# Kernel optimization log

Measured on AMD Instinct MI355X. Metric: run time of the kernel, lower is better.

Reference implementation:

```python
import jax, jax.numpy as jnp
import numpy as np

N_NODES = 100000
N_EDGES = 1600000
IN_FEAT = 64
HIDDEN = 128
N_CLASSES = 16
N_GRAPHS = 512


def _glorot(key, shape):
    fan_in, fan_out = shape
    lim = (6.0 / (fan_in + fan_out)) ** 0.5
    return jax.random.uniform(key, shape, jnp.float32, -lim, lim)


def setup_inputs() -> dict:
    key = jax.random.key(0)
    ks = jax.random.split(key, 12)
    x = jax.random.normal(ks[0], (N_NODES, IN_FEAT), jnp.float32)
    edge_index = jax.random.randint(ks[1], (2, N_EDGES), 0, N_NODES, jnp.int64)
    batch = jnp.sort(jax.random.randint(ks[2], (N_NODES,), 0, N_GRAPHS, jnp.int64))
    # SAGEConv params: lin_l (neighbor agg, with bias), lin_r (root, no bias)
    params = {}
    dims = [(IN_FEAT, HIDDEN), (HIDDEN, HIDDEN), (HIDDEN, HIDDEN)]
    for i, (din, dout) in enumerate(dims, start=1):
        params[f"Wl{i}"] = _glorot(ks[2 + 2 * i - 1], (din, dout))
        params[f"bl{i}"] = jnp.zeros((dout,), jnp.float32)
        params[f"Wr{i}"] = _glorot(ks[2 + 2 * i], (din, dout))
    params["W_out"] = _glorot(ks[9], (HIDDEN, N_CLASSES))
    params["b_out"] = jnp.zeros((N_CLASSES,), jnp.float32)
    return {"x": x, "edge_index": edge_index, "batch": batch, **params}


def _sage_conv(x, src, dst, Wl, bl, Wr):
    # mean aggregation of neighbor (source) features onto target nodes
    msg = x[src]                                                # [E, D]
    agg_sum = jax.ops.segment_sum(msg, dst, num_segments=N_NODES)
    cnt = jax.ops.segment_sum(jnp.ones((src.shape[0],), x.dtype), dst,
                              num_segments=N_NODES)
    agg = agg_sum / jnp.maximum(cnt, 1.0)[:, None]
    return agg @ Wl + bl + x @ Wr


def reference(x, edge_index, batch, Wl1, bl1, Wr1, Wl2, bl2, Wr2,
              Wl3, bl3, Wr3, W_out, b_out):
    src, dst = edge_index[0], edge_index[1]
    h = jax.nn.relu(_sage_conv(x, src, dst, Wl1, bl1, Wr1))
    h = jax.nn.relu(_sage_conv(h, src, dst, Wl2, bl2, Wr2))
    h = _sage_conv(h, src, dst, Wl3, bl3, Wr3)
    # global mean pool over graphs
    g_sum = jax.ops.segment_sum(h, batch, num_segments=N_GRAPHS)
    g_cnt = jax.ops.segment_sum(jnp.ones((h.shape[0],), h.dtype), batch,
                                num_segments=N_GRAPHS)
    g = g_sum / jnp.maximum(g_cnt, 1.0)[:, None]
    # dropout is identity at inference (module.eval())
    return g @ W_out + b_out
```

## Files before the change

kernel.cpp:

```cpp
#include <hip/hip_runtime.h>

#define N_NODES   100000
#define N_PAD     100096
#define N_EDGES   1600000
#define IN_FEAT   64
#define HIDDEN    128
#define N_CLASSES 16
#define N_GRAPHS  512
#define MAXDEG    64

#define BIN_NODES 512
#define NBINS     196
#define N_NODES_B (NBINS * BIN_NODES)
#define BINCAP    9000
#define EPB       2048

typedef __attribute__((ext_vector_type(8))) unsigned short us8;
typedef __attribute__((ext_vector_type(8))) short s8v;
typedef __attribute__((ext_vector_type(4))) float f4v;

__device__ __forceinline__ unsigned short f2bf(float f) {
    unsigned u = __builtin_bit_cast(unsigned, f);
    unsigned r = u + 0x7FFFu + ((u >> 16) & 1u);
    return (unsigned short)(r >> 16);
}
__device__ __forceinline__ float bf2f(unsigned short h) {
    unsigned u = ((unsigned)h) << 16;
    return __builtin_bit_cast(float, u);
}
__device__ __forceinline__ void acc8(float* a, us8 v) {
#pragma unroll
    for (int e = 0; e < 8; e++) a[e] += bf2f(v[e]);
}


__global__ __launch_bounds__(512) void bin_kernel(const int* __restrict__ src,
                                                  const int* __restrict__ dst,
                                                  int* __restrict__ bin_cursor,
                                                  int2* __restrict__ binbuf) {
    __shared__ int hist[NBINS];
    __shared__ int base[NBINS];
    const int t = threadIdx.x;
    for (int i = t; i < NBINS; i += 512) hist[i] = 0;
    __syncthreads();

    const int e0 = blockIdx.x * EPB;
    int myb[4], mys[4], myd[4], myp[4];
#pragma unroll
    for (int j = 0; j < 4; j++) {
        int e = e0 + t + j * 512;
        if (e < N_EDGES) {
            myd[j] = dst[e];
            mys[j] = src[e];
            myb[j] = myd[j] >> 9;
        } else {
            myb[j] = -1; mys[j] = 0; myd[j] = 0;
        }
    }
#pragma unroll
    for (int j = 0; j < 4; j++)
        myp[j] = (myb[j] >= 0) ? atomicAdd(&hist[myb[j]], 1) : 0;
    __syncthreads();

    for (int i = t; i < NBINS; i += 512) {
        int h = hist[i];
        base[i] = (h > 0) ? atomicAdd(&bin_cursor[i], h) : 0;
    }
    __syncthreads();

#pragma unroll
    for (int j = 0; j < 4; j++) {
        if (myb[j] >= 0) {
            int pos = base[myb[j]] + myp[j];
            if (pos < BINCAP)
                binbuf[(size_t)myb[j] * BINCAP + pos] = make_int2(mys[j], myd[j]);
        }
    }
}


__global__ __launch_bounds__(512) void build_kernel(const int2* __restrict__ binbuf,
                                                    const int* __restrict__ bin_cursor,
                                                    int* __restrict__ cursor,
                                                    int* __restrict__ csr) {
    __shared__ int lcur[BIN_NODES];
    __shared__ int lcsr[BIN_NODES * MAXDEG];
    const int b = blockIdx.x, t = threadIdx.x;
    if (t < BIN_NODES) lcur[t] = 0;
    __syncthreads();

    int cnt = bin_cursor[b];
    if (cnt > BINCAP) cnt = BINCAP;
    const int2* __restrict__ eb = binbuf + (size_t)b * BINCAP;
    for (int i = t; i < cnt; i += 512) {
        int2 e = eb[i];
        int dl = e.y - b * BIN_NODES;
        int p = atomicAdd(&lcur[dl], 1);
        if (p < MAXDEG) lcsr[dl * MAXDEG + p] = e.x;
    }
    __syncthreads();

    int4* __restrict__ gout = reinterpret_cast<int4*>(csr + (size_t)b * BIN_NODES * MAXDEG);
    const int4* __restrict__ lin = reinterpret_cast<const int4*>(lcsr);
    for (int i = t; i < BIN_NODES * MAXDEG / 4; i += 512) gout[i] = lin[i];
    if (t < BIN_NODES) cursor[b * BIN_NODES + t] = lcur[t];
}


__global__ void convert_x_kernel(const float* __restrict__ x, ushort* __restrict__ xh) {
    const int flat = blockIdx.x * 256 + threadIdx.x;
    const int row = flat >> 3;
    us8 w;
    if (row < N_NODES) {
        const float* p = x + (size_t)flat * 8;
        float4 v0 = *reinterpret_cast<const float4*>(p);
        float4 v1 = *reinterpret_cast<const float4*>(p + 4);
        w[0] = f2bf(v0.x); w[1] = f2bf(v0.y); w[2] = f2bf(v0.z); w[3] = f2bf(v0.w);
        w[4] = f2bf(v1.x); w[5] = f2bf(v1.y); w[6] = f2bf(v1.z); w[7] = f2bf(v1.w);
    } else {
#pragma unroll
        for (int e = 0; e < 8; e++) w[e] = 0;
    }
    reinterpret_cast<us8*>(xh)[flat] = w;
}


__global__ void pack_weights_kernel(const float* __restrict__ s0, const float* __restrict__ s1,
                                    const float* __restrict__ s2, const float* __restrict__ s3,
                                    const float* __restrict__ s4, const float* __restrict__ s5,
                                    ushort* __restrict__ Bpk) {
    const int flat = blockIdx.x * 256 + threadIdx.x;
    const float* src; int base;
    if      (flat < 8192)  { src = s0; base = 0; }
    else if (flat < 16384) { src = s1; base = 8192; }
    else if (flat < 32768) { src = s2; base = 16384; }
    else if (flat < 49152) { src = s3; base = 32768; }
    else if (flat < 65536) { src = s4; base = 49152; }
    else                   { src = s5; base = 65536; }
    const int local = flat - base;
    const int j    = local & 7;
    const int lane = (local >> 3) & 63;
    const int tile = local >> 9;
    const int ks = tile >> 3, ct = tile & 7;
    const int row = ks * 32 + ((lane >> 4) << 3) + j;
    const int col = (ct << 4) + (lane & 15);
    Bpk[flat] = f2bf(src[row * 128 + col]);
}


template <int D>
__global__ __launch_bounds__(256) void aggregate_bf(
        const ushort* __restrict__ feat, const int* __restrict__ cursor,
        const int* __restrict__ csr, ushort* __restrict__ aggout) {
    constexpr int LPN = D / 8;
    constexpr int NPB = 256 / LPN;
    const int tid  = threadIdx.x;
    const int lane = tid & (LPN - 1);
    const int n    = blockIdx.x * NPB + tid / LPN;
    if (n >= N_NODES) return;
    const int start = n * MAXDEG;
    int cnt = cursor[n];
    if (cnt > MAXDEG) cnt = MAXDEG;
    const us8* __restrict__ f8 = reinterpret_cast<const us8*>(feat);

    float a[8] = {0.f, 0.f, 0.f, 0.f, 0.f, 0.f, 0.f, 0.f};
    int i = 0;
    for (; i + 8 <= cnt; i += 8) {
        int t0 = csr[start + i + 0], t1 = csr[start + i + 1];
        int t2 = csr[start + i + 2], t3 = csr[start + i + 3];
        int t4 = csr[start + i + 4], t5 = csr[start + i + 5];
        int t6 = csr[start + i + 6], t7 = csr[start + i + 7];
        us8 v0 = f8[(size_t)t0 * LPN + lane];
        us8 v1 = f8[(size_t)t1 * LPN + lane];
        us8 v2 = f8[(size_t)t2 * LPN + lane];
        us8 v3 = f8[(size_t)t3 * LPN + lane];
        us8 v4 = f8[(size_t)t4 * LPN + lane];
        us8 v5 = f8[(size_t)t5 * LPN + lane];
        us8 v6 = f8[(size_t)t6 * LPN + lane];
        us8 v7 = f8[(size_t)t7 * LPN + lane];
        acc8(a, v0); acc8(a, v1); acc8(a, v2); acc8(a, v3);
        acc8(a, v4); acc8(a, v5); acc8(a, v6); acc8(a, v7);
    }
    for (; i + 4 <= cnt; i += 4) {
        int t0 = csr[start + i + 0], t1 = csr[start + i + 1];
        int t2 = csr[start + i + 2], t3 = csr[start + i + 3];
        us8 v0 = f8[(size_t)t0 * LPN + lane];
        us8 v1 = f8[(size_t)t1 * LPN + lane];
        us8 v2 = f8[(size_t)t2 * LPN + lane];
        us8 v3 = f8[(size_t)t3 * LPN + lane];
        acc8(a, v0); acc8(a, v1); acc8(a, v2); acc8(a, v3);
    }
    for (; i < cnt; i++) {
        us8 v0 = f8[(size_t)csr[start + i] * LPN + lane];
        acc8(a, v0);
    }
    const float inv = 1.f / (float)(cnt > 0 ? cnt : 1);
    us8 w;
#pragma unroll
    for (int e = 0; e < 8; e++) w[e] = f2bf(a[e] * inv);
    reinterpret_cast<us8*>(aggout)[(size_t)n * LPN + lane] = w;
}


template <int K, bool RELU>
__global__ __launch_bounds__(256, 2) void gemm_mfma(
        const ushort* __restrict__ A1, const ushort* __restrict__ A2,
        const ushort* __restrict__ B1p, const ushort* __restrict__ B2p,
        const float* __restrict__ bias, ushort* __restrict__ out) {
    constexpr int KS = K / 32;
    __shared__ ushort Bs[2 * KS * 8 * 512];
    const int tid = threadIdx.x;
    {
        const us8* g1 = reinterpret_cast<const us8*>(B1p);
        const us8* g2 = reinterpret_cast<const us8*>(B2p);
        us8* l8 = reinterpret_cast<us8*>(Bs);
        constexpr int PH = KS * 512;
#pragma unroll
        for (int i = 0; i < 4 * KS; i++) {
            int c = i * 256 + tid;
            if (i < 2 * KS) l8[c] = g1[c];
            else            l8[c] = g2[c - PH];
        }
    }
    __syncthreads();

    const int wave = tid >> 6, lane = tid & 63;
    const int r0 = blockIdx.x * 128 + wave * 32;
    const size_t arow = (size_t)(r0 + (lane & 15));
    const int koff = (lane >> 4) << 3;

    f4v acc[2][8];
#pragma unroll
    for (int rt = 0; rt < 2; rt++)
#pragma unroll
        for (int ct = 0; ct < 8; ct++) acc[rt][ct] = (f4v){0.f, 0.f, 0.f, 0.f};

    const s8v* Bf = reinterpret_cast<const s8v*>(Bs);
#pragma unroll
    for (int ph = 0; ph < 2; ph++) {
        const ushort* __restrict__ A = ph ? A2 : A1;
#pragma unroll
        for (int ks = 0; ks < KS; ks++) {
            s8v a0 = *reinterpret_cast<const s8v*>(A + arow * K + ks * 32 + koff);
            s8v a1 = *reinterpret_cast<const s8v*>(A + (arow + 16) * K + ks * 32 + koff);
#pragma unroll
            for (int ct = 0; ct < 8; ct++) {
                s8v b = Bf[((ph * KS + ks) * 8 + ct) * 64 + lane];
                acc[0][ct] = __builtin_amdgcn_mfma_f32_16x16x32_bf16(a0, b, acc[0][ct], 0, 0, 0);
                acc[1][ct] = __builtin_amdgcn_mfma_f32_16x16x32_bf16(a1, b, acc[1][ct], 0, 0, 0);
            }
        }
    }

    const int colb = lane & 15;
    const int rowb = (lane >> 4) << 2;
#pragma unroll
    for (int rt = 0; rt < 2; rt++) {
#pragma unroll
        for (int ct = 0; ct < 8; ct++) {
            const int col = ct * 16 + colb;
            const float bb = bias[col];
#pragma unroll
            for (int j = 0; j < 4; j++) {
                int row = r0 + rt * 16 + rowb + j;
                if (row < N_NODES) {
                    float v = acc[rt][ct][j] + bb;
                    if (RELU) v = fmaxf(v, 0.f);
                    out[(size_t)row * HIDDEN + col] = f2bf(v);
                }
            }
        }
    }
}


__global__ __launch_bounds__(256) void pool_bf(const ushort* __restrict__ h,
                                               const int* __restrict__ batch,
                                               float* __restrict__ g) {
    __shared__ int sb[5];
    const int g0 = blockIdx.x * 4;
    const int tid = threadIdx.x;
    if (tid <= 4) {
        int target = g0 + tid;
        int lo = 0, hi = N_NODES;
        while (lo < hi) {
            int mid = (lo + hi) >> 1;
            if (batch[mid] < target) lo = mid + 1; else hi = mid;
        }
        sb[tid] = lo;
    }
    __syncthreads();
    const int lg = tid >> 6;
    const int lane = tid & 63;
    const int s = sb[lg], e = sb[lg + 1];
    const int nsub = lane >> 4;
    const int cc = lane & 15;
    const us8* __restrict__ h8 = reinterpret_cast<const us8*>(h);

    float a[8] = {0.f, 0.f, 0.f, 0.f, 0.f, 0.f, 0.f, 0.f};
    int n = s + nsub;
    for (; n + 12 < e; n += 16) {
        us8 v0 = h8[(size_t)(n + 0) * 16 + cc];
        us8 v1 = h8[(size_t)(n + 4) * 16 + cc];
        us8 v2 = h8[(size_t)(n + 8) * 16 + cc];
        us8 v3 = h8[(size_t)(n + 12) * 16 + cc];
        acc8(a, v0); acc8(a, v1); acc8(a, v2); acc8(a, v3);
    }
    for (; n < e; n += 4) {
        us8 v0 = h8[(size_t)n * 16 + cc];
        acc8(a, v0);
    }
#pragma unroll
    for (int e2 = 0; e2 < 8; e2++) {
        a[e2] += __shfl_xor(a[e2], 16);
        a[e2] += __shfl_xor(a[e2], 32);
    }
    if (nsub == 0) {
        const int cnt = e - s;
        const float inv = 1.f / (float)(cnt > 0 ? cnt : 1);
        float4 w0 = make_float4(a[0] * inv, a[1] * inv, a[2] * inv, a[3] * inv);
        float4 w1 = make_float4(a[4] * inv, a[5] * inv, a[6] * inv, a[7] * inv);
        float* dst = g + (size_t)(g0 + lg) * HIDDEN + cc * 8;
        *reinterpret_cast<float4*>(dst) = w0;
        *reinterpret_cast<float4*>(dst + 4) = w1;
    }
}


__global__ void head_kernel(const float* __restrict__ g, const float* __restrict__ W,
                            const float* __restrict__ b, float* __restrict__ out) {
    const int gid = blockIdx.x * 4 + (threadIdx.x >> 4);
    const int f = threadIdx.x & 15;
    if (gid >= N_GRAPHS) return;
    float acc = b[f];
    for (int k = 0; k < HIDDEN; k++)
        acc += g[(size_t)gid * HIDDEN + k] * W[k * N_CLASSES + f];
    out[(size_t)gid * N_CLASSES + f] = acc;
}


extern "C" void kernel_launch(void* const* d_in, const int* in_sizes, int n_in,
                              void* d_out, int out_size, void* d_ws, size_t ws_size,
                              hipStream_t stream) {
    const float* x    = (const float*)d_in[0];
    const int* eidx   = (const int*)d_in[1];
    const int* batch  = (const int*)d_in[2];
    const float* Wl1  = (const float*)d_in[3];
    const float* bl1  = (const float*)d_in[4];
    const float* Wr1  = (const float*)d_in[5];
    const float* Wl2  = (const float*)d_in[6];
    const float* bl2  = (const float*)d_in[7];
    const float* Wr2  = (const float*)d_in[8];
    const float* Wl3  = (const float*)d_in[9];
    const float* bl3  = (const float*)d_in[10];
    const float* Wr3  = (const float*)d_in[11];
    const float* Wout = (const float*)d_in[12];
    const float* bout = (const float*)d_in[13];
    float* out = (float*)d_out;

    const int* esrc = eidx;
    const int* edst = eidx + N_EDGES;

    char* ws = (char*)d_ws;
    size_t o = 0;
    int*  bin_cursor = (int*)(ws + o);  o += 256 * 4;
    int*  cursor     = (int*)(ws + o);  o += (size_t)N_NODES_B * 4;
    int*  csr        = (int*)(ws + o);  o += (size_t)N_NODES_B * MAXDEG * 4;
    int2* binbuf     = (int2*)(ws + o); o += (size_t)NBINS * BINCAP * 8;
    o = (o + 255) & ~(size_t)255;
    ushort* xh   = (ushort*)(ws + o); o += (size_t)N_PAD * IN_FEAT * 2;
    ushort* aggb = (ushort*)(ws + o); o += (size_t)N_PAD * HIDDEN * 2;
    ushort* h1b  = (ushort*)(ws + o); o += (size_t)N_PAD * HIDDEN * 2;
    ushort* h2b  = (ushort*)(ws + o); o += (size_t)N_PAD * HIDDEN * 2;
    ushort* Bpk  = (ushort*)(ws + o); o += (size_t)81920 * 2;
    float*  g    = (float*)(ws + o);  o += (size_t)N_GRAPHS * HIDDEN * 4;

    hipMemsetAsync(bin_cursor, 0, 256 * 4, stream);

    bin_kernel<<<(N_EDGES + EPB - 1) / EPB, 512, 0, stream>>>(esrc, edst, bin_cursor, binbuf);
    build_kernel<<<NBINS, 512, 0, stream>>>(binbuf, bin_cursor, cursor, csr);

    pack_weights_kernel<<<320, 256, 0, stream>>>(Wl1, Wr1, Wl2, Wr2, Wl3, Wr3, Bpk);
    convert_x_kernel<<<(N_PAD * IN_FEAT / 8) / 256, 256, 0, stream>>>(x, xh);

    ushort* Wl1p = Bpk + 0,     *Wr1p = Bpk + 8192;
    ushort* Wl2p = Bpk + 16384, *Wr2p = Bpk + 32768;
    ushort* Wl3p = Bpk + 49152, *Wr3p = Bpk + 65536;

    const int GB = N_PAD / 128;

    aggregate_bf<IN_FEAT><<<(N_NODES + 31) / 32, 256, 0, stream>>>(xh, cursor, csr, aggb);
    gemm_mfma<IN_FEAT, true><<<GB, 256, 0, stream>>>(aggb, xh, Wl1p, Wr1p, bl1, h1b);
    aggregate_bf<HIDDEN><<<(N_NODES + 15) / 16, 256, 0, stream>>>(h1b, cursor, csr, aggb);
    gemm_mfma<HIDDEN, true><<<GB, 256, 0, stream>>>(aggb, h1b, Wl2p, Wr2p, bl2, h2b);
    aggregate_bf<HIDDEN><<<(N_NODES + 15) / 16, 256, 0, stream>>>(h2b, cursor, csr, aggb);
    gemm_mfma<HIDDEN, false><<<GB, 256, 0, stream>>>(aggb, h2b, Wl3p, Wr3p, bl3, h1b);

    pool_bf<<<N_GRAPHS / 4, 256, 0, stream>>>(h1b, batch, g);
    head_kernel<<<N_GRAPHS / 4, 64, 0, stream>>>(g, Wout, bout, out);
}
```

Baseline: 373.2 us.

## Fuse neighbor mean aggregation into the MFMA GEMM per layer

Removes the separate aggregate kernel and gathers neighbor features directly into MFMA A-fragments inside the GEMM kernel, producing the bf16 mean in registers. This drops the write and re-read of the aggregated buffer and three kernel launches. In exchange, each lane now gathers strided 16-byte chunks per neighbor for two rows serially, with only 2-way unrolling. That lowers memory-level parallelism and coalescing compared with the dedicated gather kernel, and register pressure goes up under launch_bounds(256,2).

```diff
diff --git a/kernel.cpp b/kernel.cpp
--- a/kernel.cpp
+++ b/kernel.cpp
@@ -148,63 +148,10 @@
 }
 
 
-template <int D>
-__global__ __launch_bounds__(256) void aggregate_bf(
-        const ushort* __restrict__ feat, const int* __restrict__ cursor,
-        const int* __restrict__ csr, ushort* __restrict__ aggout) {
-    constexpr int LPN = D / 8;
-    constexpr int NPB = 256 / LPN;
-    const int tid  = threadIdx.x;
-    const int lane = tid & (LPN - 1);
-    const int n    = blockIdx.x * NPB + tid / LPN;
-    if (n >= N_NODES) return;
-    const int start = n * MAXDEG;
-    int cnt = cursor[n];
-    if (cnt > MAXDEG) cnt = MAXDEG;
-    const us8* __restrict__ f8 = reinterpret_cast<const us8*>(feat);
-
-    float a[8] = {0.f, 0.f, 0.f, 0.f, 0.f, 0.f, 0.f, 0.f};
-    int i = 0;
-    for (; i + 8 <= cnt; i += 8) {
-        int t0 = csr[start + i + 0], t1 = csr[start + i + 1];
-        int t2 = csr[start + i + 2], t3 = csr[start + i + 3];
-        int t4 = csr[start + i + 4], t5 = csr[start + i + 5];
-        int t6 = csr[start + i + 6], t7 = csr[start + i + 7];
-        us8 v0 = f8[(size_t)t0 * LPN + lane];
-        us8 v1 = f8[(size_t)t1 * LPN + lane];
-        us8 v2 = f8[(size_t)t2 * LPN + lane];
-        us8 v3 = f8[(size_t)t3 * LPN + lane];
-        us8 v4 = f8[(size_t)t4 * LPN + lane];
-        us8 v5 = f8[(size_t)t5 * LPN + lane];
-        us8 v6 = f8[(size_t)t6 * LPN + lane];
-        us8 v7 = f8[(size_t)t7 * LPN + lane];
-        acc8(a, v0); acc8(a, v1); acc8(a, v2); acc8(a, v3);
-        acc8(a, v4); acc8(a, v5); acc8(a, v6); acc8(a, v7);
-    }
-    for (; i + 4 <= cnt; i += 4) {
-        int t0 = csr[start + i + 0], t1 = csr[start + i + 1];
-        int t2 = csr[start + i + 2], t3 = csr[start + i + 3];
-        us8 v0 = f8[(size_t)t0 * LPN + lane];
-        us8 v1 = f8[(size_t)t1 * LPN + lane];
-        us8 v2 = f8[(size_t)t2 * LPN + lane];
-        us8 v3 = f8[(size_t)t3 * LPN + lane];
-        acc8(a, v0); acc8(a, v1); acc8(a, v2); acc8(a, v3);
-    }
-    for (; i < cnt; i++) {
-        us8 v0 = f8[(size_t)csr[start + i] * LPN + lane];
-        acc8(a, v0);
-    }
-    const float inv = 1.f / (float)(cnt > 0 ? cnt : 1);
-    us8 w;
-#pragma unroll
-    for (int e = 0; e < 8; e++) w[e] = f2bf(a[e] * inv);
-    reinterpret_cast<us8*>(aggout)[(size_t)n * LPN + lane] = w;
-}
-
-
 template <int K, bool RELU>
-__global__ __launch_bounds__(256, 2) void gemm_mfma(
-        const ushort* __restrict__ A1, const ushort* __restrict__ A2,
+__global__ __launch_bounds__(256, 2) void fused_agg_gemm(
+        const ushort* __restrict__ feat,
+        const int* __restrict__ cursor, const int* __restrict__ csr,
         const ushort* __restrict__ B1p, const ushort* __restrict__ B2p,
         const float* __restrict__ bias, ushort* __restrict__ out) {
     constexpr int KS = K / 32;
@@ -226,9 +173,56 @@
 
     const int wave = tid >> 6, lane = tid & 63;
     const int r0 = blockIdx.x * 128 + wave * 32;
-    const size_t arow = (size_t)(r0 + (lane & 15));
+    const int rowbase = r0 + (lane & 15);
     const int koff = (lane >> 4) << 3;
 
+    s8v a1[2][KS];
+#pragma unroll
+    for (int rt = 0; rt < 2; rt++) {
+        const int arow = rowbase + rt * 16;
+        const int base = arow * MAXDEG;
+        int cnt = cursor[arow];
+        if (cnt > MAXDEG) cnt = MAXDEG;
+        float accf[KS][8];
+#pragma unroll
+        for (int ks = 0; ks < KS; ks++)
+#pragma unroll
+            for (int j = 0; j < 8; j++) accf[ks][j] = 0.f;
+
+        int i = 0;
+        for (; i + 2 <= cnt; i += 2) {
+            int s0 = csr[base + i], s1 = csr[base + i + 1];
+            us8 v0[KS], v1[KS];
+#pragma unroll
+            for (int ks = 0; ks < KS; ks++) {
+                v0[ks] = *reinterpret_cast<const us8*>(feat + (size_t)s0 * K + ks * 32 + koff);
+                v1[ks] = *reinterpret_cast<const us8*>(feat + (size_t)s1 * K + ks * 32 + koff);
+            }
+#pragma unroll
+            for (int ks = 0; ks < KS; ks++)
+#pragma unroll
+                for (int j = 0; j < 8; j++)
+                    accf[ks][j] += bf2f(v0[ks][j]) + bf2f(v1[ks][j]);
+        }
+        if (i < cnt) {
+            int s0 = csr[base + i];
+#pragma unroll
+            for (int ks = 0; ks < KS; ks++) {
+                us8 v0 = *reinterpret_cast<const us8*>(feat + (size_t)s0 * K + ks * 32 + koff);
+#pragma unroll
+                for (int j = 0; j < 8; j++) accf[ks][j] += bf2f(v0[j]);
+            }
+        }
+        const float inv = 1.f / (float)(cnt > 0 ? cnt : 1);
+#pragma unroll
+        for (int ks = 0; ks < KS; ks++) {
+            s8v t;
+#pragma unroll
+            for (int j = 0; j < 8; j++) t[j] = (short)f2bf(accf[ks][j] * inv);
+            a1[rt][ks] = t;
+        }
+    }
+
     f4v acc[2][8];
 #pragma unroll
     for (int rt = 0; rt < 2; rt++)
@@ -237,18 +231,23 @@
 
     const s8v* Bf = reinterpret_cast<const s8v*>(Bs);
 #pragma unroll
-    for (int ph = 0; ph < 2; ph++) {
-        const ushort* __restrict__ A = ph ? A2 : A1;
-#pragma unroll
-        for (int ks = 0; ks < KS; ks++) {
-            s8v a0 = *reinterpret_cast<const s8v*>(A + arow * K + ks * 32 + koff);
-            s8v a1 = *reinterpret_cast<const s8v*>(A + (arow + 16) * K + ks * 32 + koff);
-#pragma unroll
-            for (int ct = 0; ct < 8; ct++) {
-                s8v b = Bf[((ph * KS + ks) * 8 + ct) * 64 + lane];
-                acc[0][ct] = __builtin_amdgcn_mfma_f32_16x16x32_bf16(a0, b, acc[0][ct], 0, 0, 0);
-                acc[1][ct] = __builtin_amdgcn_mfma_f32_16x16x32_bf16(a1, b, acc[1][ct], 0, 0, 0);
-            }
+    for (int ks = 0; ks < KS; ks++) {
+#pragma unroll
+        for (int ct = 0; ct < 8; ct++) {
+            s8v b = Bf[(ks * 8 + ct) * 64 + lane];
+            acc[0][ct] = __builtin_amdgcn_mfma_f32_16x16x32_bf16(a1[0][ks], b, acc[0][ct], 0, 0, 0);
+            acc[1][ct] = __builtin_amdgcn_mfma_f32_16x16x32_bf16(a1[1][ks], b, acc[1][ct], 0, 0, 0);
+        }
+    }
+#pragma unroll
+    for (int ks = 0; ks < KS; ks++) {
+        s8v s0 = *reinterpret_cast<const s8v*>(feat + (size_t)rowbase * K + ks * 32 + koff);
+        s8v s1 = *reinterpret_cast<const s8v*>(feat + (size_t)(rowbase + 16) * K + ks * 32 + koff);
+#pragma unroll
+        for (int ct = 0; ct < 8; ct++) {
+            s8v b = Bf[((KS + ks) * 8 + ct) * 64 + lane];
+            acc[0][ct] = __builtin_amdgcn_mfma_f32_16x16x32_bf16(s0, b, acc[0][ct], 0, 0, 0);
+            acc[1][ct] = __builtin_amdgcn_mfma_f32_16x16x32_bf16(s1, b, acc[1][ct], 0, 0, 0);
         }
     }
 
@@ -369,7 +368,6 @@
     int2* binbuf     = (int2*)(ws + o); o += (size_t)NBINS * BINCAP * 8;
     o = (o + 255) & ~(size_t)255;
     ushort* xh   = (ushort*)(ws + o); o += (size_t)N_PAD * IN_FEAT * 2;
-    ushort* aggb = (ushort*)(ws + o); o += (size_t)N_PAD * HIDDEN * 2;
     ushort* h1b  = (ushort*)(ws + o); o += (size_t)N_PAD * HIDDEN * 2;
     ushort* h2b  = (ushort*)(ws + o); o += (size_t)N_PAD * HIDDEN * 2;
     ushort* Bpk  = (ushort*)(ws + o); o += (size_t)81920 * 2;
@@ -389,12 +387,9 @@
 
     const int GB = N_PAD / 128;
 
-    aggregate_bf<IN_FEAT><<<(N_NODES + 31) / 32, 256, 0, stream>>>(xh, cursor, csr, aggb);
-    gemm_mfma<IN_FEAT, true><<<GB, 256, 0, stream>>>(aggb, xh, Wl1p, Wr1p, bl1, h1b);
-    aggregate_bf<HIDDEN><<<(N_NODES + 15) / 16, 256, 0, stream>>>(h1b, cursor, csr, aggb);
-    gemm_mfma<HIDDEN, true><<<GB, 256, 0, stream>>>(aggb, h1b, Wl2p, Wr2p, bl2, h2b);
-    aggregate_bf<HIDDEN><<<(N_NODES + 15) / 16, 256, 0, stream>>>(h2b, cursor, csr, aggb);
-    gemm_mfma<HIDDEN, false><<<GB, 256, 0, stream>>>(aggb, h2b, Wl3p, Wr3p, bl3, h1b);
+    fused_agg_gemm<IN_FEAT, true><<<GB, 256, 0, stream>>>(xh, cursor, csr, Wl1p, Wr1p, bl1, h1b);
+    fused_agg_gemm<HIDDEN, true><<<GB, 256, 0, stream>>>(h1b, cursor, csr, Wl2p, Wr2p, bl2, h2b);
+    fused_agg_gemm<HIDDEN, false><<<GB, 256, 0, stream>>>(h2b, cursor, csr, Wl3p, Wr3p, bl3, h1b);
 
     pool_bf<<<N_GRAPHS / 4, 256, 0, stream>>>(h1b, batch, g);
     head_kernel<<<N_GRAPHS / 4, 64, 0, stream>>>(g, Wout, bout, out);
```

Result: slower. 414.8 us (+11.1%).

## Fuse neighbor mean aggregation into the SAGE layer MFMA GEMM via LDS

Applied to the files above, without the earlier changes.

Merges the separate aggregation and GEMM kernels into one kernel per layer. Each block gathers and averages neighbor features for its 128 rows and writes them into an XOR-swizzled LDS tile, then runs the MFMA GEMM straight from LDS. This removes the round-trip of the aggregated activations through global memory and three kernel launches. Weights are now read from global memory and no longer staged in LDS, and launch bounds rise to 4 blocks per CU. The gather phase and the MFMA phase are no longer overlapped across separate kernels, so each block must finish gathering before it computes.

```diff
diff --git a/kernel.cpp b/kernel.cpp
--- a/kernel.cpp
+++ b/kernel.cpp
@@ -148,86 +148,79 @@
 }
 
 
-template <int D>
-__global__ __launch_bounds__(256) void aggregate_bf(
-        const ushort* __restrict__ feat, const int* __restrict__ cursor,
-        const int* __restrict__ csr, ushort* __restrict__ aggout) {
-    constexpr int LPN = D / 8;
-    constexpr int NPB = 256 / LPN;
-    const int tid  = threadIdx.x;
-    const int lane = tid & (LPN - 1);
-    const int n    = blockIdx.x * NPB + tid / LPN;
-    if (n >= N_NODES) return;
-    const int start = n * MAXDEG;
-    int cnt = cursor[n];
-    if (cnt > MAXDEG) cnt = MAXDEG;
-    const us8* __restrict__ f8 = reinterpret_cast<const us8*>(feat);
-
-    float a[8] = {0.f, 0.f, 0.f, 0.f, 0.f, 0.f, 0.f, 0.f};
-    int i = 0;
-    for (; i + 8 <= cnt; i += 8) {
-        int t0 = csr[start + i + 0], t1 = csr[start + i + 1];
-        int t2 = csr[start + i + 2], t3 = csr[start + i + 3];
-        int t4 = csr[start + i + 4], t5 = csr[start + i + 5];
-        int t6 = csr[start + i + 6], t7 = csr[start + i + 7];
-        us8 v0 = f8[(size_t)t0 * LPN + lane];
-        us8 v1 = f8[(size_t)t1 * LPN + lane];
-        us8 v2 = f8[(size_t)t2 * LPN + lane];
-        us8 v3 = f8[(size_t)t3 * LPN + lane];
-        us8 v4 = f8[(size_t)t4 * LPN + lane];
-        us8 v5 = f8[(size_t)t5 * LPN + lane];
-        us8 v6 = f8[(size_t)t6 * LPN + lane];
-        us8 v7 = f8[(size_t)t7 * LPN + lane];
-        acc8(a, v0); acc8(a, v1); acc8(a, v2); acc8(a, v3);
-        acc8(a, v4); acc8(a, v5); acc8(a, v6); acc8(a, v7);
-    }
-    for (; i + 4 <= cnt; i += 4) {
-        int t0 = csr[start + i + 0], t1 = csr[start + i + 1];
-        int t2 = csr[start + i + 2], t3 = csr[start + i + 3];
-        us8 v0 = f8[(size_t)t0 * LPN + lane];
-        us8 v1 = f8[(size_t)t1 * LPN + lane];
-        us8 v2 = f8[(size_t)t2 * LPN + lane];
-        us8 v3 = f8[(size_t)t3 * LPN + lane];
-        acc8(a, v0); acc8(a, v1); acc8(a, v2); acc8(a, v3);
-    }
-    for (; i < cnt; i++) {
-        us8 v0 = f8[(size_t)csr[start + i] * LPN + lane];
-        acc8(a, v0);
-    }
-    const float inv = 1.f / (float)(cnt > 0 ? cnt : 1);
-    us8 w;
-#pragma unroll
-    for (int e = 0; e < 8; e++) w[e] = f2bf(a[e] * inv);
-    reinterpret_cast<us8*>(aggout)[(size_t)n * LPN + lane] = w;
-}
-
-
 template <int K, bool RELU>
-__global__ __launch_bounds__(256, 2) void gemm_mfma(
-        const ushort* __restrict__ A1, const ushort* __restrict__ A2,
+__global__ __launch_bounds__(256, 4) void sage_layer(
+        const ushort* __restrict__ feat,
+        const int* __restrict__ cursor, const int* __restrict__ csr,
         const ushort* __restrict__ B1p, const ushort* __restrict__ B2p,
         const float* __restrict__ bias, ushort* __restrict__ out) {
-    constexpr int KS = K / 32;
-    __shared__ ushort Bs[2 * KS * 8 * 512];
+    constexpr int KS  = K / 32;
+    constexpr int NCH = K / 8;
+    constexpr int LPN = K / 8;
+    constexpr int NPP = 256 / LPN;
+    __shared__ ushort A_lds[128 * K];
+    us8* __restrict__ A8 = reinterpret_cast<us8*>(A_lds);
+
     const int tid = threadIdx.x;
+    const int r0 = blockIdx.x * 128;
+
     {
-        const us8* g1 = reinterpret_cast<const us8*>(B1p);
-        const us8* g2 = reinterpret_cast<const us8*>(B2p);
-        us8* l8 = reinterpret_cast<us8*>(Bs);
-        constexpr int PH = KS * 512;
-#pragma unroll
-        for (int i = 0; i < 4 * KS; i++) {
-            int c = i * 256 + tid;
-            if (i < 2 * KS) l8[c] = g1[c];
-            else            l8[c] = g2[c - PH];
+        const int ch   = tid & (LPN - 1);
+        const int slot = tid / LPN;
+        const us8* __restrict__ f8 = reinterpret_cast<const us8*>(feat);
+#pragma unroll
+        for (int p = 0; p < 128 / NPP; p++) {
+            const int rl = p * NPP + slot;
+            const int n  = r0 + rl;
+            const int start = n * MAXDEG;
+            int cnt = cursor[n];
+            if (cnt > MAXDEG) cnt = MAXDEG;
+
+            float a[8] = {0.f, 0.f, 0.f, 0.f, 0.f, 0.f, 0.f, 0.f};
+            int i = 0;
+            for (; i + 8 <= cnt; i += 8) {
+                int t0 = csr[start + i + 0], t1 = csr[start + i + 1];
+                int t2 = csr[start + i + 2], t3 = csr[start + i + 3];
+                int t4 = csr[start + i + 4], t5 = csr[start + i + 5];
+                int t6 = csr[start + i + 6], t7 = csr[start + i + 7];
+                us8 v0 = f8[(size_t)t0 * LPN + ch];
+                us8 v1 = f8[(size_t)t1 * LPN + ch];
+                us8 v2 = f8[(size_t)t2 * LPN + ch];
+                us8 v3 = f8[(size_t)t3 * LPN + ch];
+                us8 v4 = f8[(size_t)t4 * LPN + ch];
+                us8 v5 = f8[(size_t)t5 * LPN + ch];
+                us8 v6 = f8[(size_t)t6 * LPN + ch];
+                us8 v7 = f8[(size_t)t7 * LPN + ch];
+                acc8(a, v0); acc8(a, v1); acc8(a, v2); acc8(a, v3);
+                acc8(a, v4); acc8(a, v5); acc8(a, v6); acc8(a, v7);
+            }
+            for (; i + 4 <= cnt; i += 4) {
+                int t0 = csr[start + i + 0], t1 = csr[start + i + 1];
+                int t2 = csr[start + i + 2], t3 = csr[start + i + 3];
+                us8 v0 = f8[(size_t)t0 * LPN + ch];
+                us8 v1 = f8[(size_t)t1 * LPN + ch];
+                us8 v2 = f8[(size_t)t2 * LPN + ch];
+                us8 v3 = f8[(size_t)t3 * LPN + ch];
+                acc8(a, v0); acc8(a, v1); acc8(a, v2); acc8(a, v3);
+            }
+            for (; i < cnt; i++) {
+                us8 v0 = f8[(size_t)csr[start + i] * LPN + ch];
+                acc8(a, v0);
+            }
+            const float inv = 1.f / (float)(cnt > 0 ? cnt : 1);
+            us8 w;
+#pragma unroll
+            for (int e = 0; e < 8; e++) w[e] = f2bf(a[e] * inv);
+            A8[rl * NCH + (ch ^ (rl & 7))] = w;
         }
     }
     __syncthreads();
 
     const int wave = tid >> 6, lane = tid & 63;
-    const int r0 = blockIdx.x * 128 + wave * 32;
-    const size_t arow = (size_t)(r0 + (lane & 15));
+    const int rw = wave * 32 + (lane & 15);
+    const int rowbase = r0 + rw;
     const int koff = (lane >> 4) << 3;
+    const int swz = rw & 7;
 
     f4v acc[2][8];
 #pragma unroll
@@ -235,20 +228,30 @@
 #pragma unroll
         for (int ct = 0; ct < 8; ct++) acc[rt][ct] = (f4v){0.f, 0.f, 0.f, 0.f};
 
-    const s8v* Bf = reinterpret_cast<const s8v*>(Bs);
-#pragma unroll
-    for (int ph = 0; ph < 2; ph++) {
-        const ushort* __restrict__ A = ph ? A2 : A1;
-#pragma unroll
-        for (int ks = 0; ks < KS; ks++) {
-            s8v a0 = *reinterpret_cast<const s8v*>(A + arow * K + ks * 32 + koff);
-            s8v a1 = *reinterpret_cast<const s8v*>(A + (arow + 16) * K + ks * 32 + koff);
-#pragma unroll
-            for (int ct = 0; ct < 8; ct++) {
-                s8v b = Bf[((ph * KS + ks) * 8 + ct) * 64 + lane];
-                acc[0][ct] = __builtin_amdgcn_mfma_f32_16x16x32_bf16(a0, b, acc[0][ct], 0, 0, 0);
-                acc[1][ct] = __builtin_amdgcn_mfma_f32_16x16x32_bf16(a1, b, acc[1][ct], 0, 0, 0);
-            }
+    const s8v* __restrict__ Als = reinterpret_cast<const s8v*>(A_lds);
+    const s8v* __restrict__ Bf1 = reinterpret_cast<const s8v*>(B1p);
+    const s8v* __restrict__ Bf2 = reinterpret_cast<const s8v*>(B2p);
+#pragma unroll
+    for (int ks = 0; ks < KS; ks++) {
+        const int c0 = ks * 4 + (lane >> 4);
+        s8v a0 = Als[rw * NCH + (c0 ^ swz)];
+        s8v a1 = Als[(rw + 16) * NCH + (c0 ^ swz)];
+#pragma unroll
+        for (int ct = 0; ct < 8; ct++) {
+            s8v b = Bf1[(ks * 8 + ct) * 64 + lane];
+            acc[0][ct] = __builtin_amdgcn_mfma_f32_16x16x32_bf16(a0, b, acc[0][ct], 0, 0, 0);
+            acc[1][ct] = __builtin_amdgcn_mfma_f32_16x16x32_bf16(a1, b, acc[1][ct], 0, 0, 0);
+        }
+    }
+#pragma unroll
+    for (int ks = 0; ks < KS; ks++) {
+        s8v s0 = *reinterpret_cast<const s8v*>(feat + (size_t)rowbase * K + ks * 32 + koff);
+        s8v s1 = *reinterpret_cast<const s8v*>(feat + (size_t)(rowbase + 16) * K + ks * 32 + koff);
+#pragma unroll
+        for (int ct = 0; ct < 8; ct++) {
+            s8v b = Bf2[(ks * 8 + ct) * 64 + lane];
+            acc[0][ct] = __builtin_amdgcn_mfma_f32_16x16x32_bf16(s0, b, acc[0][ct], 0, 0, 0);
+            acc[1][ct] = __builtin_amdgcn_mfma_f32_16x16x32_bf16(s1, b, acc[1][ct], 0, 0, 0);
         }
     }
 
@@ -262,7 +265,7 @@
             const float bb = bias[col];
 #pragma unroll
             for (int j = 0; j < 4; j++) {
-                int row = r0 + rt * 16 + rowb + j;
+                int row = r0 + wave * 32 + rt * 16 + rowb + j;
                 if (row < N_NODES) {
                     float v = acc[rt][ct][j] + bb;
                     if (RELU) v = fmaxf(v, 0.f);
@@ -369,7 +372,6 @@
     int2* binbuf     = (int2*)(ws + o); o += (size_t)NBINS * BINCAP * 8;
     o = (o + 255) & ~(size_t)255;
     ushort* xh   = (ushort*)(ws + o); o += (size_t)N_PAD * IN_FEAT * 2;
-    ushort* aggb = (ushort*)(ws + o); o += (size_t)N_PAD * HIDDEN * 2;
     ushort* h1b  = (ushort*)(ws + o); o += (size_t)N_PAD * HIDDEN * 2;
     ushort* h2b  = (ushort*)(ws + o); o += (size_t)N_PAD * HIDDEN * 2;
     ushort* Bpk  = (ushort*)(ws + o); o += (size_t)81920 * 2;
@@ -389,12 +391,9 @@
 
     const int GB = N_PAD / 128;
 
-    aggregate_bf<IN_FEAT><<<(N_NODES + 31) / 32, 256, 0, stream>>>(xh, cursor, csr, aggb);
-    gemm_mfma<IN_FEAT, true><<<GB, 256, 0, stream>>>(aggb, xh, Wl1p, Wr1p, bl1, h1b);
-    aggregate_bf<HIDDEN><<<(N_NODES + 15) / 16, 256, 0, stream>>>(h1b, cursor, csr, aggb);
-    gemm_mfma<HIDDEN, true><<<GB, 256, 0, stream>>>(aggb, h1b, Wl2p, Wr2p, bl2, h2b);
-    aggregate_bf<HIDDEN><<<(N_NODES + 15) / 16, 256, 0, stream>>>(h2b, cursor, csr, aggb);
-    gemm_mfma<HIDDEN, false><<<GB, 256, 0, stream>>>(aggb, h2b, Wl3p, Wr3p, bl3, h1b);
+    sage_layer<IN_FEAT, true><<<GB, 256, 0, stream>>>(xh, cursor, csr, Wl1p, Wr1p, bl1, h1b);
+    sage_layer<HIDDEN, true><<<GB, 256, 0, stream>>>(h1b, cursor, csr, Wl2p, Wr2p, bl2, h2b);
+    sage_layer<HIDDEN, false><<<GB, 256, 0, stream>>>(h2b, cursor, csr, Wl3p, Wr3p, bl3, h1b);
 
     pool_bf<<<N_GRAPHS / 4, 256, 0, stream>>>(h1b, batch, g);
     head_kernel<<<N_GRAPHS / 4, 64, 0, stream>>>(g, Wout, bout, out);
```

Result: no change. 373.6 us (+0.1%).
